# Kernel tuning notes

Hardware: AMD Instinct MI355X
Metric: run time of the kernel (lower is better)

## Reference

```python
import jax, jax.numpy as jnp
import numpy as np

L, DIM, H, DH, MUL = 4, 1024, 16, 64, 4
INNER = H * DH
HID = DIM * MUL
EPS = 1e-5


def setup_inputs() -> dict:
    key = jax.random.key(0)
    ks = jax.random.split(key, 16)
    s = 0.02
    inp = {
        "x": jax.random.normal(ks[0], (2, 2048, DIM), dtype=jnp.float32),
        "ln1_g": jnp.ones((L, DIM), jnp.float32),
        "ln1_b": jnp.zeros((L, DIM), jnp.float32),
        "Wq": jax.random.normal(ks[1], (L, DIM, INNER), jnp.float32) * s,
        "Wk": jax.random.normal(ks[2], (L, DIM, INNER), jnp.float32) * s,
        "Wv": jax.random.normal(ks[3], (L, DIM, INNER), jnp.float32) * s,
        "Wo": jax.random.normal(ks[4], (L, INNER, DIM), jnp.float32) * s,
        "ln3_g": jnp.ones((L, DIM), jnp.float32),
        "ln3_b": jnp.zeros((L, DIM), jnp.float32),
        "fc1_w": jax.random.normal(ks[5], (L, DIM, HID), jnp.float32) * s,
        "fc1_b": jnp.zeros((L, HID), jnp.float32),
        "fc2_w": jax.random.normal(ks[6], (L, HID, DIM), jnp.float32) * s,
        "fc2_b": jnp.zeros((L, DIM), jnp.float32),
    }
    return inp


def _layernorm(x, g, b):
    mu = jnp.mean(x, axis=-1, keepdims=True)
    var = jnp.var(x, axis=-1, keepdims=True)
    return (x - mu) * jax.lax.rsqrt(var + EPS) * g + b


def _attention(xn, wq, wk, wv, wo):
    B, S, _ = xn.shape
    q = (xn @ wq).reshape(B, S, H, DH).transpose(0, 2, 1, 3)  # b h s d
    k = (xn @ wk).reshape(B, S, H, DH).transpose(0, 2, 1, 3)
    v = (xn @ wv).reshape(B, S, H, DH).transpose(0, 2, 1, 3)
    scale = DH ** -0.5
    sim = jnp.einsum("bhid,bhjd->bhij", q, k) * scale
    mask = jnp.triu(jnp.ones((S, S), dtype=bool), k=1)
    sim = jnp.where(mask, jnp.finfo(sim.dtype).min, sim)
    attn = jax.nn.softmax(sim, axis=-1)
    out = jnp.einsum("bhij,bhjd->bhid", attn, v)
    out = out.transpose(0, 2, 1, 3).reshape(B, S, INNER)
    return out @ wo


def reference(x, ln1_g, ln1_b, Wq, Wk, Wv, Wo, ln3_g, ln3_b, fc1_w, fc1_b, fc2_w, fc2_b):
    for l in range(L):
        x = x + _attention(_layernorm(x, ln1_g[l], ln1_b[l]), Wq[l], Wk[l], Wv[l], Wo[l])
        h = _layernorm(x, ln3_g[l], ln3_b[l])
        h = jax.nn.gelu(h @ fc1_w[l] + fc1_b[l], approximate=False)
        x = x + (h @ fc2_w[l] + fc2_b[l])
    return x
```

## Files before the change

### kernel.cpp

```cpp
#include <hip/hip_runtime.h>

typedef unsigned short u16;
typedef unsigned int u32;
typedef __attribute__((ext_vector_type(8))) short short8;
typedef __attribute__((ext_vector_type(4))) float f32x4;
typedef __attribute__((ext_vector_type(4))) unsigned short u16x4;

__device__ inline u16 f2bf(float f) {
  u32 u = __builtin_bit_cast(u32, f);
  u32 r = (u + 0x7fffu + ((u >> 16) & 1u)) >> 16;
  return (u16)r;
}

__device__ inline void gload16(const void* g, void* l) {
  __builtin_amdgcn_global_load_lds((const __attribute__((address_space(1))) void*)g,
                                   (__attribute__((address_space(3))) void*)l, 16, 0, 0);
}

__global__ __launch_bounds__(256) void transpose_cast(
    const float* __restrict__ src, u16* __restrict__ dst, int K, int N,
    size_t sstride, size_t dstride)
{
  src += (size_t)blockIdx.z * sstride;
  dst += (size_t)blockIdx.z * dstride;
  __shared__ u16 tile[64][72];
  int bk = blockIdx.x * 64, bn = blockIdx.y * 64;
  int t = threadIdx.x;
  int r = t >> 2, c0 = (t & 3) * 16;
  const float* sp = src + (size_t)(bk + r) * N + bn + c0;
#pragma unroll
  for (int j = 0; j < 16; j += 4) {
    float4 v = *(const float4*)(sp + j);
    tile[r][c0 + j + 0] = f2bf(v.x);
    tile[r][c0 + j + 1] = f2bf(v.y);
    tile[r][c0 + j + 2] = f2bf(v.z);
    tile[r][c0 + j + 3] = f2bf(v.w);
  }
  __syncthreads();
  int nr = t >> 2, k0 = (t & 3) * 16;
  u16* dp = dst + (size_t)(bn + nr) * K + bk + k0;
  short8 v0, v1;
#pragma unroll
  for (int j = 0; j < 8; ++j) v0[j] = (short)tile[k0 + j][nr];
#pragma unroll
  for (int j = 0; j < 8; ++j) v1[j] = (short)tile[k0 + 8 + j][nr];
  *(short8*)dp = v0;
  *(short8*)(dp + 8) = v1;
}

__global__ __launch_bounds__(256) void vtranspose(
    const u16* __restrict__ qkv, u16* __restrict__ vtb)
{
  __shared__ u16 tile[64][72];
  int bt = blockIdx.x;
  int bh = blockIdx.y;
  int b = bh >> 4, h = bh & 15;
  const u16* src = qkv + (size_t)b * 2048 * 3072 + 2048 + h * 64;
  u16* dst = vtb + (size_t)bh * 64 * 2048;
  int t = threadIdx.x;
  int r = t >> 2, c0 = (t & 3) * 16;
  const u16* sp = src + (size_t)(bt * 64 + r) * 3072 + c0;
  *(short8*)&tile[r][c0] = *(const short8*)sp;
  *(short8*)&tile[r][c0 + 8] = *(const short8*)(sp + 8);
  __syncthreads();
  int nr = t >> 2, k0 = (t & 3) * 16;
  u16* dp = dst + (size_t)nr * 2048 + bt * 64 + k0;
  short8 v0, v1;
#pragma unroll
  for (int j = 0; j < 8; ++j) v0[j] = (short)tile[k0 + j][nr];
#pragma unroll
  for (int j = 0; j < 8; ++j) v1[j] = (short)tile[k0 + 8 + j][nr];
  *(short8*)dp = v0;
  *(short8*)(dp + 8) = v1;
}

__global__ __launch_bounds__(256) void ln_kernel(
    const float* __restrict__ x, const float* __restrict__ g,
    const float* __restrict__ be, u16* __restrict__ out)
{
  int row = blockIdx.x;
  int t = threadIdx.x;
  const float4* xr = (const float4*)(x + (size_t)row * 1024);
  float4 v = xr[t];
  float s = v.x + v.y + v.z + v.w;
  float ss = v.x * v.x + v.y * v.y + v.z * v.z + v.w * v.w;
#pragma unroll
  for (int off = 1; off < 64; off <<= 1) {
    s += __shfl_xor(s, off);
    ss += __shfl_xor(ss, off);
  }
  __shared__ float red[8];
  int w = t >> 6, lane = t & 63;
  if (lane == 0) { red[w * 2] = s; red[w * 2 + 1] = ss; }
  __syncthreads();
  s = red[0] + red[2] + red[4] + red[6];
  ss = red[1] + red[3] + red[5] + red[7];
  float mu = s * (1.0f / 1024.0f);
  float var = ss * (1.0f / 1024.0f) - mu * mu;
  float rs = rsqrtf(var + 1e-5f);
  float4 gg = ((const float4*)g)[t];
  float4 bb = ((const float4*)be)[t];
  u16x4 o;
  o[0] = f2bf((v.x - mu) * rs * gg.x + bb.x);
  o[1] = f2bf((v.y - mu) * rs * gg.y + bb.y);
  o[2] = f2bf((v.z - mu) * rs * gg.z + bb.z);
  o[3] = f2bf((v.w - mu) * rs * gg.w + bb.w);
  ((u16x4*)(out + (size_t)row * 1024))[t] = o;
}

template <int EPI, int BN>
__global__ __launch_bounds__(256) void gemm_bf16(
    const u16* __restrict__ A, const u16* __restrict__ Bt,
    u16* __restrict__ C, const float* __restrict__ bias, float* X,
    int M, int N, int K)
{
  constexpr int NJ = BN / 32;
  __shared__ __align__(16) u16 As[2][128 * 32];
  __shared__ __align__(16) u16 Bs[2][BN * 32];
  int bm = blockIdx.x * 128, bn = blockIdx.y * BN;
  int klen = K / gridDim.z;
  int kbeg = blockIdx.z * klen;
  int tid = threadIdx.x;
  int w = tid >> 6, lane = tid & 63;
  int wm = (w >> 1) * 64, wn = (w & 1) * (BN / 2);
  int frow = lane & 15, fkb = lane >> 4;

  f32x4 acc[4][NJ];
#pragma unroll
  for (int i = 0; i < 4; ++i)
#pragma unroll
    for (int j = 0; j < NJ; ++j) acc[i][j] = (f32x4){0.f, 0.f, 0.f, 0.f};

  int ca0 = tid, ca1 = tid + 256;
  int ar0 = ca0 >> 2, ak0 = (((ca0 & 3) ^ ((ar0 >> 1) & 3))) * 8;
  int ar1 = ca1 >> 2, ak1 = (((ca1 & 3) ^ ((ar1 >> 1) & 3))) * 8;
  const u16* Abase = A + (size_t)bm * K;
  const u16* Bbase = Bt + (size_t)bn * K;

  int offa[4], offb[NJ];
#pragma unroll
  for (int i = 0; i < 4; ++i) {
    int row = wm + i * 16 + frow;
    offa[i] = row * 32 + ((fkb ^ ((row >> 1) & 3)) * 8);
  }
#pragma unroll
  for (int j = 0; j < NJ; ++j) {
    int row = wn + j * 16 + frow;
    offb[j] = row * 32 + ((fkb ^ ((row >> 1) & 3)) * 8);
  }

  int nt = klen >> 5;

#define STAGE(buf, k0)                                                              \
  do {                                                                              \
    gload16(Abase + (size_t)ar0 * K + (k0) + ak0, &As[buf][(size_t)(w * 64) * 8]);  \
    gload16(Abase + (size_t)ar1 * K + (k0) + ak1, &As[buf][(size_t)(256 + w * 64) * 8]); \
    gload16(Bbase + (size_t)ar0 * K + (k0) + ak0, &Bs[buf][(size_t)(w * 64) * 8]);  \
    if constexpr (BN == 128)                                                        \
      gload16(Bbase + (size_t)ar1 * K + (k0) + ak1, &Bs[buf][(size_t)(256 + w * 64) * 8]); \
  } while (0)

  STAGE(0, kbeg);
  __syncthreads();
  int cur = 0;
  for (int t = 0; t < nt; ++t) {
    if (t + 1 < nt) STAGE(cur ^ 1, kbeg + (t + 1) * 32);
    short8 a[4], b[NJ];
#pragma unroll
    for (int i = 0; i < 4; ++i) a[i] = *(const short8*)&As[cur][offa[i]];
#pragma unroll
    for (int j = 0; j < NJ; ++j) b[j] = *(const short8*)&Bs[cur][offb[j]];
#pragma unroll
    for (int i = 0; i < 4; ++i)
#pragma unroll
      for (int j = 0; j < NJ; ++j)
        acc[i][j] = __builtin_amdgcn_mfma_f32_16x16x32_bf16(a[i], b[j], acc[i][j], 0, 0, 0);
    __syncthreads();
    cur ^= 1;
  }
#undef STAGE

  int r0 = (lane >> 4) * 4;
#pragma unroll
  for (int i = 0; i < 4; ++i) {
#pragma unroll
    for (int r = 0; r < 4; ++r) {
      int gr = bm + wm + i * 16 + r0 + r;
      size_t rowb = (size_t)gr * N;
#pragma unroll
      for (int j = 0; j < NJ; ++j) {
        int gc = bn + wn + j * 16 + frow;
        float v = acc[i][j][r];
        if constexpr (EPI == 0) {
          C[rowb + gc] = f2bf(v);
        } else if constexpr (EPI == 1) {
          v += bias[gc];
          v = 0.5f * v * (1.0f + erff(v * 0.70710678118654752f));
          C[rowb + gc] = f2bf(v);
        } else if constexpr (EPI == 2) {
          if (bias) v += bias[gc];
          X[rowb + gc] += v;
        } else {
          if (kbeg == 0 && bias) v += bias[gc];
          atomicAdd(&X[rowb + gc], v);
        }
      }
    }
  }
}

__global__ __launch_bounds__(256) void flash_attn4(
    const u16* __restrict__ qkv, const u16* __restrict__ vtb, u16* __restrict__ ao)
{
  const int SEQ = 2048, LDQ = 3072;
  const float SCL2 = 0.18033688011112042f;
  int ib = blockIdx.x;
  int qb = (ib < 256) ? (15 - (ib >> 5)) : ((ib - 256) >> 5);
  int bh = ib & 31;
  int b = bh >> 4, h = bh & 15;
  size_t base = (size_t)b * SEQ * LDQ;
  const u16* Qp = qkv + base + h * 64;
  const u16* Kp = qkv + base + 1024 + h * 64;
  const u16* Vtp = vtb + (size_t)bh * 64 * SEQ;

  __shared__ __align__(16) u16 Kt[64][72];
  __shared__ __align__(16) u16 Vt[64][72];
  __shared__ __align__(16) u16 Pl[4][32][72];

  int tid = threadIdx.x;
  int w = tid >> 6, lane = tid & 63;
  int frow = lane & 15, fkh = lane >> 4;
  int fk = fkh * 8;
  int qbase = qb * 128 + w * 32;

  short8 qf[2][2];
#pragma unroll
  for (int qi = 0; qi < 2; ++qi) {
    const u16* qr = Qp + (size_t)(qbase + qi * 16 + frow) * LDQ;
    qf[qi][0] = *(const short8*)(qr + fk);
    qf[qi][1] = *(const short8*)(qr + 32 + fk);
  }

  short8 ones;
#pragma unroll
  for (int j = 0; j < 8; ++j) ones[j] = (short)0x3F80;

  f32x4 o[2][4];
  f32x4 lacc[2];
#pragma unroll
  for (int qi = 0; qi < 2; ++qi) {
    lacc[qi] = (f32x4){0.f, 0.f, 0.f, 0.f};
#pragma unroll
    for (int nf = 0; nf < 4; ++nf) o[qi][nf] = (f32x4){0.f, 0.f, 0.f, 0.f};
  }

  int sr0 = tid >> 3, sc0 = (tid & 7) * 8;
  int sr1 = (tid + 256) >> 3, sc1 = ((tid + 256) & 7) * 8;

  int ntiles = qb * 2 + 2;

  short8 kr0 = *(const short8*)(Kp + (size_t)sr0 * LDQ + sc0);
  short8 kr1 = *(const short8*)(Kp + (size_t)sr1 * LDQ + sc1);
  short8 vr0 = *(const short8*)(Vtp + (size_t)sr0 * SEQ + sc0);
  short8 vr1 = *(const short8*)(Vtp + (size_t)sr1 * SEQ + sc1);

  for (int jb = 0; jb < ntiles; ++jb) {
    __syncthreads();
    *(short8*)&Kt[sr0][sc0] = kr0;
    *(short8*)&Kt[sr1][sc1] = kr1;
    *(short8*)&Vt[sr0][sc0] = vr0;
    *(short8*)&Vt[sr1][sc1] = vr1;
    __syncthreads();

    if (jb + 1 < ntiles) {
      kr0 = *(const short8*)(Kp + (size_t)((jb + 1) * 64 + sr0) * LDQ + sc0);
      kr1 = *(const short8*)(Kp + (size_t)((jb + 1) * 64 + sr1) * LDQ + sc1);
      vr0 = *(const short8*)(Vtp + (size_t)sr0 * SEQ + (jb + 1) * 64 + sc0);
      vr1 = *(const short8*)(Vtp + (size_t)sr1 * SEQ + (jb + 1) * 64 + sc1);
    }

    short8 kf[4][2];
#pragma unroll
    for (int nf = 0; nf < 4; ++nf) {
      kf[nf][0] = *(const short8*)&Kt[nf * 16 + frow][fk];
      kf[nf][1] = *(const short8*)&Kt[nf * 16 + frow][32 + fk];
    }

#pragma unroll
    for (int qi = 0; qi < 2; ++qi) {
      f32x4 s[4];
#pragma unroll
      for (int nf = 0; nf < 4; ++nf) s[nf] = (f32x4){0.f, 0.f, 0.f, 0.f};
#pragma unroll
      for (int nf = 0; nf < 4; ++nf) {
        s[nf] = __builtin_amdgcn_mfma_f32_16x16x32_bf16(qf[qi][0], kf[nf][0], s[nf], 0, 0, 0);
        s[nf] = __builtin_amdgcn_mfma_f32_16x16x32_bf16(qf[qi][1], kf[nf][1], s[nf], 0, 0, 0);
      }

      float pv[4][4];
#pragma unroll
      for (int nf = 0; nf < 4; ++nf)
#pragma unroll
        for (int r = 0; r < 4; ++r) pv[nf][r] = s[nf][r] * SCL2;

      bool needmask = (jb * 64 + 63) > (qbase + qi * 16);
      if (needmask) {
#pragma unroll
        for (int nf = 0; nf < 4; ++nf)
#pragma unroll
          for (int r = 0; r < 4; ++r) {
            int tok = jb * 64 + nf * 16 + frow;
            int qr = qbase + qi * 16 + fkh * 4 + r;
            if (tok > qr) pv[nf][r] = -1e30f;
          }
      }

#pragma unroll
      for (int nf = 0; nf < 4; ++nf)
#pragma unroll
        for (int r = 0; r < 4; ++r) {
          float p = exp2f(pv[nf][r]);
          Pl[w][qi * 16 + fkh * 4 + r][nf * 16 + frow] = f2bf(p);
        }
    }

    asm volatile("s_waitcnt lgkmcnt(0)" ::: "memory");
#pragma unroll
    for (int ks = 0; ks < 2; ++ks) {
      short8 pa0 = *(const short8*)&Pl[w][frow][ks * 32 + fk];
      short8 pa1 = *(const short8*)&Pl[w][16 + frow][ks * 32 + fk];
      lacc[0] = __builtin_amdgcn_mfma_f32_16x16x32_bf16(pa0, ones, lacc[0], 0, 0, 0);
      lacc[1] = __builtin_amdgcn_mfma_f32_16x16x32_bf16(pa1, ones, lacc[1], 0, 0, 0);
#pragma unroll
      for (int nf = 0; nf < 4; ++nf) {
        short8 vb = *(const short8*)&Vt[nf * 16 + frow][ks * 32 + fk];
        o[0][nf] = __builtin_amdgcn_mfma_f32_16x16x32_bf16(pa0, vb, o[0][nf], 0, 0, 0);
        o[1][nf] = __builtin_amdgcn_mfma_f32_16x16x32_bf16(pa1, vb, o[1][nf], 0, 0, 0);
      }
    }
  }

#pragma unroll
  for (int qi = 0; qi < 2; ++qi) {
    float inv[4];
#pragma unroll
    for (int r = 0; r < 4; ++r) inv[r] = 1.0f / lacc[qi][r];
#pragma unroll
    for (int nf = 0; nf < 4; ++nf) {
#pragma unroll
      for (int r = 0; r < 4; ++r) {
        int qr = qbase + qi * 16 + fkh * 4 + r;
        int dc = nf * 16 + frow;
        ao[((size_t)b * SEQ + qr) * 1024 + h * 64 + dc] = f2bf(o[qi][nf][r] * inv[r]);
      }
    }
  }
}

extern "C" void kernel_launch(void* const* d_in, const int* in_sizes, int n_in,
                              void* d_out, int out_size, void* d_ws, size_t ws_size,
                              hipStream_t stream)
{
  const float* x_in = (const float*)d_in[0];
  const float* ln1g = (const float*)d_in[1];
  const float* ln1b = (const float*)d_in[2];
  const float* Wq   = (const float*)d_in[3];
  const float* Wk   = (const float*)d_in[4];
  const float* Wv   = (const float*)d_in[5];
  const float* Wo   = (const float*)d_in[6];
  const float* ln3g = (const float*)d_in[7];
  const float* ln3b = (const float*)d_in[8];
  const float* fc1w = (const float*)d_in[9];
  const float* fc1b = (const float*)d_in[10];
  const float* fc2w = (const float*)d_in[11];
  const float* fc2b = (const float*)d_in[12];

  float* xbuf = (float*)d_out;

  char* ws = (char*)d_ws;
  size_t off = 0;
  u16* xn     = (u16*)(ws + off);  off += (size_t)4096 * 1024 * 2;
  u16* qkvb   = (u16*)(ws + off);  off += (size_t)4096 * 3072 * 2;
  u16* aob    = (u16*)(ws + off);  off += (size_t)4096 * 1024 * 2;
  u16* hbuf   = qkvb;
  u16* vtb    = (u16*)(ws + off);  off += (size_t)32 * 64 * 2048 * 2;
  u16* wqkv   = (u16*)(ws + off);  off += (size_t)4 * 3072 * 1024 * 2;
  u16* wo_t   = (u16*)(ws + off);  off += (size_t)4 * 1024 * 1024 * 2;
  u16* wfc1   = (u16*)(ws + off);  off += (size_t)4 * 4096 * 1024 * 2;
  u16* wfc2   = (u16*)(ws + off);  off += (size_t)4 * 1024 * 4096 * 2;

  hipMemcpyAsync(xbuf, x_in, (size_t)4096 * 1024 * 4, hipMemcpyDeviceToDevice, stream);

  dim3 blk(256);
  const size_t W1 = (size_t)1024 * 1024;
  transpose_cast<<<dim3(16, 16, 4), blk, 0, stream>>>(Wq, wqkv,                 1024, 1024, W1, (size_t)3072 * 1024);
  transpose_cast<<<dim3(16, 16, 4), blk, 0, stream>>>(Wk, wqkv + W1,            1024, 1024, W1, (size_t)3072 * 1024);
  transpose_cast<<<dim3(16, 16, 4), blk, 0, stream>>>(Wv, wqkv + 2 * W1,        1024, 1024, W1, (size_t)3072 * 1024);
  transpose_cast<<<dim3(16, 16, 4), blk, 0, stream>>>(Wo, wo_t,                 1024, 1024, W1, W1);
  transpose_cast<<<dim3(16, 64, 4), blk, 0, stream>>>(fc1w, wfc1,               1024, 4096, (size_t)4096 * 1024, (size_t)4096 * 1024);
  transpose_cast<<<dim3(64, 16, 4), blk, 0, stream>>>(fc2w, wfc2,               4096, 1024, (size_t)4096 * 1024, (size_t)4096 * 1024);

  for (int l = 0; l < 4; ++l) {
    ln_kernel<<<4096, blk, 0, stream>>>(xbuf, ln1g + l * 1024, ln1b + l * 1024, xn);
    gemm_bf16<0, 128><<<dim3(32, 24), blk, 0, stream>>>(xn, wqkv + (size_t)l * 3072 * 1024, qkvb, nullptr, nullptr, 4096, 3072, 1024);
    vtranspose<<<dim3(32, 32), blk, 0, stream>>>(qkvb, vtb);
    flash_attn4<<<dim3(512), blk, 0, stream>>>(qkvb, vtb, aob);
    gemm_bf16<2, 64><<<dim3(32, 16), blk, 0, stream>>>(aob, wo_t + (size_t)l * 1024 * 1024, nullptr, nullptr, xbuf, 4096, 1024, 1024);
    ln_kernel<<<4096, blk, 0, stream>>>(xbuf, ln3g + l * 1024, ln3b + l * 1024, xn);
    gemm_bf16<1, 128><<<dim3(32, 32), blk, 0, stream>>>(xn, wfc1 + (size_t)l * 4096 * 1024, hbuf, fc1b + l * 4096, nullptr, 4096, 4096, 1024);
    gemm_bf16<3, 64><<<dim3(32, 16, 2), blk, 0, stream>>>(hbuf, wfc2 + (size_t)l * 1024 * 4096, nullptr, fc2b + l * 1024, xbuf, 4096, 1024, 4096);
  }
}
```

Before: 1.128 ms.

## Replace atomic split-K fc2 GEMM with intra-block split-K LDS reduction

The fc2 GEMM (K=4096) previously split K across two grid z-slices and combined the partial sums with float atomicAdd into the residual. A new 512-thread kernel gives each half of the K range to a group of four waves inside one block. The two halves are reduced through LDS scratch and written with a plain read-add-store, which removes the atomics. The block is now twice as large, which can lower occupancy, and the scratch reuse of the As buffers must fit the accumulator size.

```diff
diff --git a/kernel.cpp b/kernel.cpp
--- a/kernel.cpp
+++ b/kernel.cpp
@@ -209,6 +209,114 @@
   }
 }
 
+template <int BN>
+__global__ __launch_bounds__(512) void gemm_bf16_sk2(
+    const u16* __restrict__ A, const u16* __restrict__ Bt,
+    const float* __restrict__ bias, float* __restrict__ X,
+    int M, int N, int K)
+{
+  constexpr int NJ = BN / 32;
+  __shared__ __align__(16) u16 As[2][2][128 * 32];
+  __shared__ __align__(16) u16 Bs[2][2][BN * 32];
+  int bm = blockIdx.x * 128, bn = blockIdx.y * BN;
+  int tid = threadIdx.x;
+  int w = tid >> 6;
+  int grp = w >> 2;
+  int wq = w & 3;
+  int lane = tid & 63;
+  int tidg = tid & 255;
+  int wm = (wq >> 1) * 64, wn = (wq & 1) * (BN / 2);
+  int frow = lane & 15, fkb = lane >> 4;
+
+  int khalf = K >> 1;
+  int kbeg = grp * khalf;
+
+  f32x4 acc[4][NJ];
+#pragma unroll
+  for (int i = 0; i < 4; ++i)
+#pragma unroll
+    for (int j = 0; j < NJ; ++j) acc[i][j] = (f32x4){0.f, 0.f, 0.f, 0.f};
+
+  int ca0 = tidg, ca1 = tidg + 256;
+  int ar0 = ca0 >> 2, ak0 = (((ca0 & 3) ^ ((ar0 >> 1) & 3))) * 8;
+  int ar1 = ca1 >> 2, ak1 = (((ca1 & 3) ^ ((ar1 >> 1) & 3))) * 8;
+  const u16* Abase = A + (size_t)bm * K;
+  const u16* Bbase = Bt + (size_t)bn * K;
+
+  int offa[4], offb[NJ];
+#pragma unroll
+  for (int i = 0; i < 4; ++i) {
+    int row = wm + i * 16 + frow;
+    offa[i] = row * 32 + ((fkb ^ ((row >> 1) & 3)) * 8);
+  }
+#pragma unroll
+  for (int j = 0; j < NJ; ++j) {
+    int row = wn + j * 16 + frow;
+    offb[j] = row * 32 + ((fkb ^ ((row >> 1) & 3)) * 8);
+  }
+
+  int nt = khalf >> 5;
+
+#define STAGE2(buf, k0)                                                                   \
+  do {                                                                                    \
+    gload16(Abase + (size_t)ar0 * K + (k0) + ak0, &As[grp][buf][(size_t)(wq * 64) * 8]);  \
+    gload16(Abase + (size_t)ar1 * K + (k0) + ak1, &As[grp][buf][(size_t)(256 + wq * 64) * 8]); \
+    gload16(Bbase + (size_t)ar0 * K + (k0) + ak0, &Bs[grp][buf][(size_t)(wq * 64) * 8]);  \
+    if constexpr (BN == 128)                                                              \
+      gload16(Bbase + (size_t)ar1 * K + (k0) + ak1, &Bs[grp][buf][(size_t)(256 + wq * 64) * 8]); \
+  } while (0)
+
+  STAGE2(0, kbeg);
+  __syncthreads();
+  int cur = 0;
+  for (int t = 0; t < nt; ++t) {
+    if (t + 1 < nt) STAGE2(cur ^ 1, kbeg + (t + 1) * 32);
+    short8 a[4], b[NJ];
+#pragma unroll
+    for (int i = 0; i < 4; ++i) a[i] = *(const short8*)&As[grp][cur][offa[i]];
+#pragma unroll
+    for (int j = 0; j < NJ; ++j) b[j] = *(const short8*)&Bs[grp][cur][offb[j]];
+#pragma unroll
+    for (int i = 0; i < 4; ++i)
+#pragma unroll
+      for (int j = 0; j < NJ; ++j)
+        acc[i][j] = __builtin_amdgcn_mfma_f32_16x16x32_bf16(a[i], b[j], acc[i][j], 0, 0, 0);
+    __syncthreads();
+    cur ^= 1;
+  }
+#undef STAGE2
+
+  float* scr = (float*)&As[0][0][0];
+  if (grp == 1) {
+#pragma unroll
+    for (int i = 0; i < 4; ++i)
+#pragma unroll
+      for (int j = 0; j < NJ; ++j)
+#pragma unroll
+        for (int r = 0; r < 4; ++r)
+          scr[(size_t)((i * NJ + j) * 4 + r) * 256 + wq * 64 + lane] = acc[i][j][r];
+  }
+  __syncthreads();
+  if (grp == 0) {
+    int r0 = (lane >> 4) * 4;
+#pragma unroll
+    for (int i = 0; i < 4; ++i) {
+#pragma unroll
+      for (int r = 0; r < 4; ++r) {
+        int gr = bm + wm + i * 16 + r0 + r;
+        size_t rowb = (size_t)gr * N;
+#pragma unroll
+        for (int j = 0; j < NJ; ++j) {
+          int gc = bn + wn + j * 16 + frow;
+          float v = acc[i][j][r] + scr[(size_t)((i * NJ + j) * 4 + r) * 256 + wq * 64 + lane];
+          if (bias) v += bias[gc];
+          X[rowb + gc] += v;
+        }
+      }
+    }
+  }
+}
+
 __global__ __launch_bounds__(256) void flash_attn4(
     const u16* __restrict__ qkv, const u16* __restrict__ vtb, u16* __restrict__ ao)
 {
@@ -408,6 +516,6 @@
     gemm_bf16<2, 64><<<dim3(32, 16), blk, 0, stream>>>(aob, wo_t + (size_t)l * 1024 * 1024, nullptr, nullptr, xbuf, 4096, 1024, 1024);
     ln_kernel<<<4096, blk, 0, stream>>>(xbuf, ln3g + l * 1024, ln3b + l * 1024, xn);
     gemm_bf16<1, 128><<<dim3(32, 32), blk, 0, stream>>>(xn, wfc1 + (size_t)l * 4096 * 1024, hbuf, fc1b + l * 4096, nullptr, 4096, 4096, 1024);
-    gemm_bf16<3, 64><<<dim3(32, 16, 2), blk, 0, stream>>>(hbuf, wfc2 + (size_t)l * 1024 * 4096, nullptr, fc2b + l * 1024, xbuf, 4096, 1024, 4096);
-  }
-}
+    gemm_bf16_sk2<64><<<dim3(32, 16), dim3(512), 0, stream>>>(hbuf, wfc2 + (size_t)l * 1024 * 4096, fc2b + l * 1024, xbuf, 4096, 1024, 4096);
+  }
+}
```

Result: no change. 1.122 ms (-0.5%).
